# Kernel tuning notes

Measured on AMD Instinct MI355X. Metric: run time of the kernel, lower is better.

Reference implementation:

```python
import jax, jax.numpy as jnp
import numpy as np
import math

B, S, F, H, E = 2, 1024, 512, 2048, 8
EPS = 1e-10

def setup_inputs() -> dict:
    key = jax.random.key(0)
    ks = jax.random.split(key, 6)
    s1 = math.sqrt(1.0 / (F + H))  # complex_xavier_init std for F->H
    s2 = math.sqrt(1.0 / (H + F))  # std for H->F
    return {
        'x_r': jax.random.normal(ks[0], (B, S, F), jnp.float32),
        'x_i': jax.random.normal(ks[1], (B, S, F), jnp.float32),
        'Wr1': jax.random.normal(ks[2], (E, F, H), jnp.float32) * s1,
        'Wi1': jax.random.normal(ks[3], (E, F, H), jnp.float32) * s1,
        'br1': jnp.zeros((E, H), jnp.float32),
        'bi1': jnp.zeros((E, H), jnp.float32),
        'mb': jnp.zeros((E, H), jnp.float32),  # ModReLU bias
        'Wr2': jax.random.normal(ks[4], (E, H, F), jnp.float32) * s2,
        'Wi2': jax.random.normal(ks[5], (E, H, F), jnp.float32) * s2,
        'br2': jnp.zeros((E, F), jnp.float32),
        'bi2': jnp.zeros((E, F), jnp.float32),
    }

def reference(x_r, x_i, Wr1, Wi1, br1, bi1, mb, Wr2, Wi2, br2, bi2):
    n_exp = Wr1.shape[0]
    # --- PhaseRouter: deterministic top-1 routing by mean token phase ---
    phase = jnp.arctan2(x_i, x_r)                      # angle(x), (B,S,F)
    mean_cos = jnp.mean(jnp.cos(phase), axis=-1)
    mean_sin = jnp.mean(jnp.sin(phase), axis=-1)
    token_phase = jnp.arctan2(mean_sin, mean_cos)      # (B,S)
    norm_phase = (token_phase + jnp.pi) / (2 * jnp.pi)
    idx = jnp.clip(jnp.floor(norm_phase * n_exp).astype(jnp.int32), 0, n_exp - 1)
    probs = jax.nn.one_hot(idx, n_exp, dtype=x_r.dtype)  # (B,S,E)
    # --- dense all-expert complex MLP (as in source: every expert on every token) ---
    # layer 1: complex linear F->H, per expert
    h_r = (jnp.einsum('bsf,efh->ebsh', x_r, Wr1) - jnp.einsum('bsf,efh->ebsh', x_i, Wi1)
           + br1[:, None, None, :])
    h_i = (jnp.einsum('bsf,efh->ebsh', x_r, Wi1) + jnp.einsum('bsf,efh->ebsh', x_i, Wr1)
           + bi1[:, None, None, :])
    # ModReLU: relu(|z|+b) * z/(|z|+eps)
    amp = jnp.sqrt(h_r * h_r + h_i * h_i + EPS)
    scale = jax.nn.relu(amp + mb[:, None, None, :]) / (amp + EPS)
    h_r = scale * h_r
    h_i = scale * h_i
    # layer 2: complex linear H->F, per expert
    y_r = (jnp.einsum('ebsh,ehf->ebsf', h_r, Wr2) - jnp.einsum('ebsh,ehf->ebsf', h_i, Wi2)
           + br2[:, None, None, :])
    y_i = (jnp.einsum('ebsh,ehf->ebsf', h_r, Wi2) + jnp.einsum('ebsh,ehf->ebsf', h_i, Wr2)
           + bi2[:, None, None, :])
    # combine: expert_weight * mask == probs * probs (one-hot, 0/1)
    w = probs * probs                                   # (B,S,E)
    out_r = jnp.einsum('ebsf,bse->bsf', y_r, w)
    out_i = jnp.einsum('ebsf,bse->bsf', y_i, w)
    return jnp.stack([out_r, out_i])                    # (2,B,S,F): real, imag
```

## Files before the change

kernel.cpp:

```cpp
#include <hip/hip_runtime.h>
#include <hip/hip_bf16.h>

#define TOKENS 2048
#define FDIM 512
#define HDIM 2048
#define NEXP 8
#define PI_F 3.14159265358979323846f

typedef __attribute__((ext_vector_type(8))) short bf16x8;
typedef __attribute__((ext_vector_type(4))) float f32x4;

__device__ __forceinline__ unsigned short f2bf(float f) {
  unsigned int u = __float_as_uint(f);
  unsigned int r = (u + 0x7fffu + ((u >> 16) & 1u)) >> 16;
  return (unsigned short)r;
}

__device__ __forceinline__ void gload16(const void* g, void* l) {
  __builtin_amdgcn_global_load_lds(
      (const __attribute__((address_space(1))) unsigned int*)g,
      (__attribute__((address_space(3))) unsigned int*)l, 16, 0, 0);
}

template<int K, int N>
__device__ __forceinline__ void pack_w_body64(
    const float* __restrict__ Wr, const float* __restrict__ Wi,
    short* __restrict__ Wp, int b, float (*tr)[33], float (*ti)[33])
{
  constexpr int NT_ = N / 32;
  int per_e = (K / 64) * NT_;
  int e = b / per_e;
  int rem = b % per_e;
  int k0 = (rem / NT_) * 64, n0 = (rem % NT_) * 32;
  int tid = threadIdx.x;
  int row = tid >> 2, c8 = (tid & 3) * 8;
  const float* wr = Wr + ((size_t)e * K + k0 + row) * N + n0 + c8;
  const float* wi = Wi + ((size_t)e * K + k0 + row) * N + n0 + c8;
  float4 a0 = *(const float4*)(wr);
  float4 a1 = *(const float4*)(wr + 4);
  float4 b0 = *(const float4*)(wi);
  float4 b1 = *(const float4*)(wi + 4);
  *(float4*)&tr[row][c8] = a0;  *(float4*)&tr[row][c8 + 4] = a1;
  *(float4*)&ti[row][c8] = b0;  *(float4*)&ti[row][c8 + 4] = b1;
  __syncthreads();
  int nl = tid >> 3, k8 = (tid & 7) * 8;
  unsigned short pr[8], pi[8];
  #pragma unroll
  for (int j = 0; j < 8; ++j) {
    pr[j] = f2bf(tr[k8 + j][nl]);
    pi[j] = f2bf(ti[k8 + j][nl]);
  }
  size_t d0 = (((size_t)e * 2 + 0) * N + n0 + nl) * K + k0 + k8;
  size_t d1 = (((size_t)e * 2 + 1) * N + n0 + nl) * K + k0 + k8;
  *(int4*)(Wp + d0) = *(const int4*)pr;
  *(int4*)(Wp + d1) = *(const int4*)pi;
}

__global__ __launch_bounds__(256) void route_packw_kernel(
    const float* __restrict__ xr, const float* __restrict__ xi,
    int* __restrict__ idx, int* __restrict__ counts,
    const float* __restrict__ Wr1, const float* __restrict__ Wi1,
    const float* __restrict__ Wr2, const float* __restrict__ Wi2,
    short* __restrict__ W1p, short* __restrict__ W2p)
{
  __shared__ float tr[64][33], ti[64][33];
  int bid = blockIdx.x;
  if (bid < 256) {
    int tid = threadIdx.x;
    int t = bid * 8 + (tid >> 5);
    int l = tid & 31;
    const float* r  = xr + (size_t)t * FDIM;
    const float* im = xi + (size_t)t * FDIM;
    float sc = 0.f, ss = 0.f;
    #pragma unroll
    for (int p = 0; p < 4; ++p) {
      int f = p * 128 + l * 4;
      float4 a4 = *(const float4*)(r + f);
      float4 b4 = *(const float4*)(im + f);
      float av[4] = {a4.x, a4.y, a4.z, a4.w};
      float bv[4] = {b4.x, b4.y, b4.z, b4.w};
      #pragma unroll
      for (int j = 0; j < 4; ++j) {
        float h2 = av[j] * av[j] + bv[j] * bv[j];
        if (h2 > 0.f) {
          float rs = rsqrtf(h2);
          sc += av[j] * rs;
          ss += bv[j] * rs;
        } else {
          sc += 1.f;
        }
      }
    }
    #pragma unroll
    for (int off = 16; off > 0; off >>= 1) {
      sc += __shfl_down(sc, off, 32);
      ss += __shfl_down(ss, off, 32);
    }
    if (l == 0) {
      float phase = atan2f(ss, sc);
      float norm = (phase + PI_F) / (2.f * PI_F);
      int e = (int)floorf(norm * (float)NEXP);
      e = min(max(e, 0), NEXP - 1);
      idx[t] = e;
      atomicAdd(&counts[e], 1);
    }
  } else {
    int b = bid - 256;
    if (b < 4096) pack_w_body64<FDIM, HDIM>(Wr1, Wi1, W1p, b, tr, ti);
    else          pack_w_body64<HDIM, FDIM>(Wr2, Wi2, W2p, b - 4096, tr, ti);
  }
}

__global__ __launch_bounds__(256) void scatter_kernel(
    const int* __restrict__ idx, const int* __restrict__ counts,
    int* __restrict__ offs, int* __restrict__ perm, int* __restrict__ rexp)
{
  __shared__ int base_e[NEXP];
  __shared__ int tcnt[256][NEXP];
  int tid = threadIdx.x;
  if (tid == 0) {
    int acc = 0;
    for (int e = 0; e < NEXP; ++e) { base_e[e] = acc; offs[e] = acc; acc += counts[e]; }
  }
  int t0 = tid * 8;
  int eo[8];
  int loc[NEXP];
  #pragma unroll
  for (int e = 0; e < NEXP; ++e) loc[e] = 0;
  #pragma unroll
  for (int j = 0; j < 8; ++j) { eo[j] = idx[t0 + j]; loc[eo[j]]++; }
  #pragma unroll
  for (int e = 0; e < NEXP; ++e) tcnt[tid][e] = loc[e];
  __syncthreads();
  if (tid < NEXP) {
    int e = tid, run = 0;
    for (int i = 0; i < 256; ++i) { int v = tcnt[i][e]; tcnt[i][e] = run; run += v; }
  }
  __syncthreads();
  #pragma unroll
  for (int e = 0; e < NEXP; ++e) loc[e] = base_e[e] + tcnt[tid][e];
  #pragma unroll
  for (int j = 0; j < 8; ++j) {
    int e = eo[j];
    int pos = loc[e]++;
    perm[pos] = t0 + j;
    rexp[pos] = e;
  }
}

__global__ __launch_bounds__(256) void pack_x_kernel(
    const float* __restrict__ xr, const float* __restrict__ xi,
    const int* __restrict__ perm,
    short* __restrict__ Ar, short* __restrict__ Ai)
{
  int gid = blockIdx.x * 256 + threadIdx.x;
  int i = gid >> 7;
  int c4 = (gid & 127) * 4;
  int tok = perm[i];
  float4 r = *(const float4*)(xr + (size_t)tok * FDIM + c4);
  float4 m = *(const float4*)(xi + (size_t)tok * FDIM + c4);
  unsigned short orr[4] = { f2bf(r.x), f2bf(r.y), f2bf(r.z), f2bf(r.w) };
  unsigned short oii[4] = { f2bf(m.x), f2bf(m.y), f2bf(m.z), f2bf(m.w) };
  *(int2*)(Ar + (size_t)i * FDIM + c4) = *(const int2*)orr;
  *(int2*)(Ai + (size_t)i * FDIM + c4) = *(const int2*)oii;
}

template<int LDK, int NC, int NX, bool IS_L1>
__global__ __launch_bounds__(256) void gemm_cplx(
    const short* __restrict__ Apr, const short* __restrict__ Api,
    const short* __restrict__ Wp,
    const int* __restrict__ counts, const int* __restrict__ offs,
    const float* __restrict__ bre, const float* __restrict__ bim,
    const float* __restrict__ mb,
    short* __restrict__ Or, short* __restrict__ Oi,
    unsigned int* __restrict__ P)
{
  constexpr int KT = 16;
  int bid = blockIdx.x;
  int virt = (bid & 7) * 256 + (bid >> 3);
  int e = virt >> 8, rem = virt & 255;
  int x = rem % NX;
  int q = rem / NX;
  int y = q & 7, s = q >> 3;
  int cnt = counts[e];
  int row0 = y * 64;
  if (row0 >= cnt) return;
  int base = offs[e];
  int n0c = x * 64;
  int kbase = s * 512;

  __shared__ __align__(16) short As[2][2][64][32];
  __shared__ __align__(16) short Ws[2][2][64][32];

  int tid = threadIdx.x;
  int lane = tid & 63;
  int w = tid >> 6, wm = w >> 1, wn = w & 1;
  int lr = lane & 15, g = lane >> 4;
  int ssw = g ^ ((lr >> 1) & 3);

  int srl = tid >> 2, slt = tid & 3;
  int sc = (slt ^ ((srl >> 1) & 3)) * 16;
  int arow = min(row0 + srl, cnt - 1);
  const char* pAr = (const char*)(Apr + (size_t)(base + arow) * LDK + kbase) + sc;
  const char* pAi = (const char*)(Api + (size_t)(base + arow) * LDK + kbase) + sc;
  const short* We = Wp + (size_t)e * 2 * NC * LDK;
  const char* pW0 = (const char*)(We + (size_t)(n0c + srl) * LDK + kbase) + sc;
  const char* pW1 = (const char*)(We + ((size_t)NC + n0c + srl) * LDK + kbase) + sc;

  auto STAGE = [&](int buf, int t) {
    char* ab = (char*)&As[0][0][0][0] + buf * 8192;
    gload16(pAr + t * 64, ab + tid * 16);
    gload16(pAi + t * 64, ab + 4096 + tid * 16);
    char* wb = (char*)&Ws[0][0][0][0] + buf * 8192;
    gload16(pW0 + t * 64, wb + tid * 16);
    gload16(pW1 + t * 64, wb + 4096 + tid * 16);
  };

  f32x4 accr[2][2], acci[2][2];
  #pragma unroll
  for (int m = 0; m < 2; ++m)
    #pragma unroll
    for (int n = 0; n < 2; ++n) { accr[m][n] = 0.f; acci[m][n] = 0.f; }

  const bf16x8 SGN = {(short)0x8000, (short)0x8000, (short)0x8000, (short)0x8000,
                      (short)0x8000, (short)0x8000, (short)0x8000, (short)0x8000};

  auto COMPUTE = [&](int buf) {
    const short* Ab = &As[0][0][0][0] + buf * 4096;
    const short* Wb = &Ws[0][0][0][0] + buf * 4096;
    bf16x8 ar[2], ai[2], wr[2], wi[2], wni[2];
    #pragma unroll
    for (int m = 0; m < 2; ++m) {
      int off = (wm * 32 + m * 16 + lr) * 32 + ssw * 8;
      ar[m] = *(const bf16x8*)(Ab + off);
      ai[m] = *(const bf16x8*)(Ab + 2048 + off);
    }
    #pragma unroll
    for (int n = 0; n < 2; ++n) {
      int offw = (wn * 32 + n * 16 + lr) * 32 + ssw * 8;
      wr[n] = *(const bf16x8*)(Wb + offw);
      wi[n] = *(const bf16x8*)(Wb + 2048 + offw);
      wni[n] = wi[n] ^ SGN;
    }
    #pragma unroll
    for (int m = 0; m < 2; ++m)
      #pragma unroll
      for (int n = 0; n < 2; ++n) {
        accr[m][n] = __builtin_amdgcn_mfma_f32_16x16x32_bf16(ar[m], wr[n],  accr[m][n], 0, 0, 0);
        accr[m][n] = __builtin_amdgcn_mfma_f32_16x16x32_bf16(ai[m], wni[n], accr[m][n], 0, 0, 0);
        acci[m][n] = __builtin_amdgcn_mfma_f32_16x16x32_bf16(ar[m], wi[n],  acci[m][n], 0, 0, 0);
        acci[m][n] = __builtin_amdgcn_mfma_f32_16x16x32_bf16(ai[m], wr[n],  acci[m][n], 0, 0, 0);
      }
  };

  STAGE(0, 0);
  int cur = 0;
  for (int t = 0; t < KT; ++t) {
    __syncthreads();
    if (t + 1 < KT) STAGE(cur ^ 1, t + 1);
    COMPUTE(cur);
    cur ^= 1;
  }

  #pragma unroll
  for (int m = 0; m < 2; ++m) {
    #pragma unroll
    for (int qq = 0; qq < 4; ++qq) {
      int row = row0 + wm * 32 + m * 16 + g * 4 + qq;
      if (row >= cnt) continue;
      #pragma unroll
      for (int n = 0; n < 2; ++n) {
        int c = n0c + wn * 32 + n * 16 + lr;
        if constexpr (IS_L1) {
          float hr = accr[m][n][qq] + bre[e * NC + c];
          float hi = acci[m][n][qq] + bim[e * NC + c];
          float s2 = hr * hr + hi * hi + 1e-10f;
          float rr = __frsqrt_rn(s2);
          float amp = s2 * rr;
          float scl = fmaxf(amp + mb[e * NC + c], 0.f) * rr;
          Or[(size_t)(base + row) * NC + c] = (short)f2bf(hr * scl);
          Oi[(size_t)(base + row) * NC + c] = (short)f2bf(hi * scl);
        } else {
          unsigned pv = (unsigned)f2bf(accr[m][n][qq])
                      | ((unsigned)f2bf(acci[m][n][qq]) << 16);
          P[((size_t)s * TOKENS + base + row) * 512 + c] = pv;
        }
      }
    }
  }
}

__global__ __launch_bounds__(256) void finalize_kernel(
    const unsigned int* __restrict__ P, const float* __restrict__ br2,
    const float* __restrict__ bi2, const int* __restrict__ perm,
    const int* __restrict__ rexp, float* __restrict__ out)
{
  int gid = blockIdx.x * 256 + threadIdx.x;
  int i = gid >> 7;
  int c4 = (gid & 127) * 4;
  float sr[4] = {0.f, 0.f, 0.f, 0.f}, si[4] = {0.f, 0.f, 0.f, 0.f};
  #pragma unroll
  for (int s = 0; s < 4; ++s) {
    uint4 u = *(const uint4*)(P + ((size_t)s * TOKENS + i) * 512 + c4);
    unsigned uv[4] = {u.x, u.y, u.z, u.w};
    #pragma unroll
    for (int j = 0; j < 4; ++j) {
      sr[j] += __uint_as_float(uv[j] << 16);
      si[j] += __uint_as_float(uv[j] & 0xFFFF0000u);
    }
  }
  int e = rexp[i], tok = perm[i];
  float4 br = *(const float4*)(br2 + e * FDIM + c4);
  float4 bi = *(const float4*)(bi2 + e * FDIM + c4);
  float4 vr = {sr[0] + br.x, sr[1] + br.y, sr[2] + br.z, sr[3] + br.w};
  float4 vi = {si[0] + bi.x, si[1] + bi.y, si[2] + bi.z, si[3] + bi.w};
  *(float4*)(out + (size_t)tok * FDIM + c4) = vr;
  *(float4*)(out + (size_t)TOKENS * FDIM + (size_t)tok * FDIM + c4) = vi;
}

extern "C" void kernel_launch(void* const* d_in, const int* in_sizes, int n_in,
                              void* d_out, int out_size, void* d_ws, size_t ws_size,
                              hipStream_t stream)
{
  const float* xr  = (const float*)d_in[0];
  const float* xi  = (const float*)d_in[1];
  const float* Wr1 = (const float*)d_in[2];
  const float* Wi1 = (const float*)d_in[3];
  const float* br1 = (const float*)d_in[4];
  const float* bi1 = (const float*)d_in[5];
  const float* mb  = (const float*)d_in[6];
  const float* Wr2 = (const float*)d_in[7];
  const float* Wi2 = (const float*)d_in[8];
  const float* br2 = (const float*)d_in[9];
  const float* bi2 = (const float*)d_in[10];
  float* out = (float*)d_out;

  char* ws = (char*)d_ws;
  int* counts = (int*)(ws + 0);
  int* offs   = (int*)(ws + 64);
  int* idx    = (int*)(ws + 128);
  int* perm   = (int*)(ws + 8320);
  int* rexp   = (int*)(ws + 16512);

  size_t off = 32768;
  short* A1r = (short*)(ws + off); off += (size_t)TOKENS * FDIM * 2;
  short* A1i = (short*)(ws + off); off += (size_t)TOKENS * FDIM * 2;
  short* A2r = (short*)(ws + off); off += (size_t)TOKENS * HDIM * 2;
  short* A2i = (short*)(ws + off); off += (size_t)TOKENS * HDIM * 2;
  short* W1p = (short*)(ws + off); off += (size_t)NEXP * 2 * HDIM * FDIM * 2;
  short* W2p = (short*)(ws + off); off += (size_t)NEXP * 2 * FDIM * HDIM * 2;
  unsigned int* P = (unsigned int*)(ws + off);

  hipMemsetAsync(counts, 0, 64, stream);
  route_packw_kernel<<<256 + 8192, 256, 0, stream>>>(
      xr, xi, idx, counts, Wr1, Wi1, Wr2, Wi2, W1p, W2p);
  scatter_kernel<<<1, 256, 0, stream>>>(idx, counts, offs, perm, rexp);
  pack_x_kernel<<<TOKENS * 128 / 256, 256, 0, stream>>>(xr, xi, perm, A1r, A1i);

  gemm_cplx<FDIM, HDIM, 32, true><<<2048, 256, 0, stream>>>(
      A1r, A1i, W1p, counts, offs, br1, bi1, mb, A2r, A2i, nullptr);
  gemm_cplx<HDIM, FDIM, 8, false><<<2048, 256, 0, stream>>>(
      A2r, A2i, W2p, counts, offs, nullptr, nullptr, nullptr, nullptr, nullptr, P);

  finalize_kernel<<<TOKENS * 128 / 256, 256, 0, stream>>>(
      P, br2, bi2, perm, rexp, out);
}
```

Measured before the change: 128.2 us.

## Overlap layer-2 weight packing with the layer-1 expert GEMM

Moves packing of the second-layer weights out of the routing kernel and into the layer-1 GEMM launch. Blocks are interleaved so one in three runs the GEMM tile and two pack W2 tiles, letting memory-bound packing overlap compute-bound GEMM work. The GEMM body becomes a device function that receives a shared-memory pointer and a passed-in XCD index. This shortens the critical path through routing and scatter, but the XCD mapping changes (bid&7 with g=bid/3), which may alter L2 locality, and many GEMM blocks exit early for experts with few tokens.

Measured after the change: 125.0 us. 1.03x faster.

```diff
diff --git a/kernel.cpp b/kernel.cpp
--- a/kernel.cpp
+++ b/kernel.cpp
@@ -56,12 +56,11 @@
   *(int4*)(Wp + d1) = *(const int4*)pi;
 }
 
-__global__ __launch_bounds__(256) void route_packw_kernel(
+__global__ __launch_bounds__(256) void route_packw1_kernel(
     const float* __restrict__ xr, const float* __restrict__ xi,
     int* __restrict__ idx, int* __restrict__ counts,
     const float* __restrict__ Wr1, const float* __restrict__ Wi1,
-    const float* __restrict__ Wr2, const float* __restrict__ Wi2,
-    short* __restrict__ W1p, short* __restrict__ W2p)
+    short* __restrict__ W1p)
 {
   __shared__ float tr[64][33], ti[64][33];
   int bid = blockIdx.x;
@@ -105,9 +104,7 @@
       atomicAdd(&counts[e], 1);
     }
   } else {
-    int b = bid - 256;
-    if (b < 4096) pack_w_body64<FDIM, HDIM>(Wr1, Wi1, W1p, b, tr, ti);
-    else          pack_w_body64<HDIM, FDIM>(Wr2, Wi2, W2p, b - 4096, tr, ti);
+    pack_w_body64<FDIM, HDIM>(Wr1, Wi1, W1p, bid - 256, tr, ti);
   }
 }
 
@@ -166,7 +163,8 @@
 }
 
 template<int LDK, int NC, int NX, bool IS_L1>
-__global__ __launch_bounds__(256) void gemm_cplx(
+__device__ __forceinline__ void gemm_body(
+    int gbid, int xcd, short* AsB, short* WsB,
     const short* __restrict__ Apr, const short* __restrict__ Api,
     const short* __restrict__ Wp,
     const int* __restrict__ counts, const int* __restrict__ offs,
@@ -176,8 +174,7 @@
     unsigned int* __restrict__ P)
 {
   constexpr int KT = 16;
-  int bid = blockIdx.x;
-  int virt = (bid & 7) * 256 + (bid >> 3);
+  int virt = xcd * 256 + (gbid >> 3);
   int e = virt >> 8, rem = virt & 255;
   int x = rem % NX;
   int q = rem / NX;
@@ -189,9 +186,6 @@
   int n0c = x * 64;
   int kbase = s * 512;
 
-  __shared__ __align__(16) short As[2][2][64][32];
-  __shared__ __align__(16) short Ws[2][2][64][32];
-
   int tid = threadIdx.x;
   int lane = tid & 63;
   int w = tid >> 6, wm = w >> 1, wn = w & 1;
@@ -208,10 +202,10 @@
   const char* pW1 = (const char*)(We + ((size_t)NC + n0c + srl) * LDK + kbase) + sc;
 
   auto STAGE = [&](int buf, int t) {
-    char* ab = (char*)&As[0][0][0][0] + buf * 8192;
+    char* ab = (char*)AsB + buf * 8192;
     gload16(pAr + t * 64, ab + tid * 16);
     gload16(pAi + t * 64, ab + 4096 + tid * 16);
-    char* wb = (char*)&Ws[0][0][0][0] + buf * 8192;
+    char* wb = (char*)WsB + buf * 8192;
     gload16(pW0 + t * 64, wb + tid * 16);
     gload16(pW1 + t * 64, wb + 4096 + tid * 16);
   };
@@ -226,8 +220,8 @@
                       (short)0x8000, (short)0x8000, (short)0x8000, (short)0x8000};
 
   auto COMPUTE = [&](int buf) {
-    const short* Ab = &As[0][0][0][0] + buf * 4096;
-    const short* Wb = &Ws[0][0][0][0] + buf * 4096;
+    const short* Ab = AsB + buf * 4096;
+    const short* Wb = WsB + buf * 4096;
     bf16x8 ar[2], ai[2], wr[2], wi[2], wni[2];
     #pragma unroll
     for (int m = 0; m < 2; ++m) {
@@ -290,6 +284,46 @@
   }
 }
 
+__global__ __launch_bounds__(256) void gemm1_packw2_kernel(
+    const short* __restrict__ A1r, const short* __restrict__ A1i,
+    const short* __restrict__ W1p,
+    const int* __restrict__ counts, const int* __restrict__ offs,
+    const float* __restrict__ br1, const float* __restrict__ bi1,
+    const float* __restrict__ mb,
+    short* __restrict__ A2r, short* __restrict__ A2i,
+    const float* __restrict__ Wr2, const float* __restrict__ Wi2,
+    short* __restrict__ W2p)
+{
+  __shared__ __align__(16) short As[2][2][64][32];
+  __shared__ __align__(16) short Ws[2][2][64][32];
+  int bid = blockIdx.x;
+  int r3 = bid % 3;
+  if (r3 == 0) {
+    int g = bid / 3;
+    gemm_body<FDIM, HDIM, 32, true>(g, bid & 7, &As[0][0][0][0], &Ws[0][0][0][0],
+        A1r, A1i, W1p, counts, offs, br1, bi1, mb, A2r, A2i, nullptr);
+  } else {
+    int pb = (bid / 3) * 2 + (r3 - 1);
+    float (*tr)[33] = (float (*)[33])&As[0][0][0][0];
+    float (*ti)[33] = (float (*)[33])&Ws[0][0][0][0];
+    pack_w_body64<HDIM, FDIM>(Wr2, Wi2, W2p, pb, tr, ti);
+  }
+}
+
+__global__ __launch_bounds__(256) void gemm2_kernel(
+    const short* __restrict__ A2r, const short* __restrict__ A2i,
+    const short* __restrict__ W2p,
+    const int* __restrict__ counts, const int* __restrict__ offs,
+    unsigned int* __restrict__ P)
+{
+  __shared__ __align__(16) short As[2][2][64][32];
+  __shared__ __align__(16) short Ws[2][2][64][32];
+  int bid = blockIdx.x;
+  gemm_body<HDIM, FDIM, 8, false>(bid, bid & 7, &As[0][0][0][0], &Ws[0][0][0][0],
+      A2r, A2i, W2p, counts, offs, nullptr, nullptr, nullptr,
+      nullptr, nullptr, P);
+}
+
 __global__ __launch_bounds__(256) void finalize_kernel(
     const unsigned int* __restrict__ P, const float* __restrict__ br2,
     const float* __restrict__ bi2, const int* __restrict__ perm,
@@ -352,15 +386,14 @@
   unsigned int* P = (unsigned int*)(ws + off);
 
   hipMemsetAsync(counts, 0, 64, stream);
-  route_packw_kernel<<<256 + 8192, 256, 0, stream>>>(
-      xr, xi, idx, counts, Wr1, Wi1, Wr2, Wi2, W1p, W2p);
+  route_packw1_kernel<<<256 + 4096, 256, 0, stream>>>(
+      xr, xi, idx, counts, Wr1, Wi1, W1p);
   scatter_kernel<<<1, 256, 0, stream>>>(idx, counts, offs, perm, rexp);
   pack_x_kernel<<<TOKENS * 128 / 256, 256, 0, stream>>>(xr, xi, perm, A1r, A1i);
 
-  gemm_cplx<FDIM, HDIM, 32, true><<<2048, 256, 0, stream>>>(
-      A1r, A1i, W1p, counts, offs, br1, bi1, mb, A2r, A2i, nullptr);
-  gemm_cplx<HDIM, FDIM, 8, false><<<2048, 256, 0, stream>>>(
-      A2r, A2i, W2p, counts, offs, nullptr, nullptr, nullptr, nullptr, nullptr, P);
+  gemm1_packw2_kernel<<<6144, 256, 0, stream>>>(
+      A1r, A1i, W1p, counts, offs, br1, bi1, mb, A2r, A2i, Wr2, Wi2, W2p);
+  gemm2_kernel<<<2048, 256, 0, stream>>>(A2r, A2i, W2p, counts, offs, P);
 
   finalize_kernel<<<TOKENS * 128 / 256, 256, 0, stream>>>(
       P, br2, bi2, perm, rexp, out);
```
